# Kernel tuning notes

Measured on AMD Instinct MI355X. Metric: run time of the kernel, lower is better.

Reference implementation:

```python
import jax, jax.numpy as jnp
import numpy as np

N_NODES = 50000
N_EDGES = 800000
IN_FEAT = 128
OUT_FEAT = 128


def setup_inputs() -> dict:
    key = jax.random.key(0)
    k_h, k_src, k_dst, k_w, k_b = jax.random.split(key, 5)
    h = jax.random.normal(k_h, (N_NODES, IN_FEAT), dtype=jnp.float32)
    src = jax.random.randint(k_src, (N_EDGES,), 0, N_NODES, dtype=jnp.int64)
    dst = jax.random.randint(k_dst, (N_EDGES,), 0, N_NODES, dtype=jnp.int64)
    # nn.Linear(2*in_feat, out_feat): weight [out, 2*in], bias [out]
    W = jax.random.normal(k_w, (OUT_FEAT, 2 * IN_FEAT), dtype=jnp.float32) / np.sqrt(2 * IN_FEAT)
    b = jax.random.normal(k_b, (OUT_FEAT,), dtype=jnp.float32) * 0.01
    return {"h": h, "src": src, "dst": dst, "W": W, "b": b}


def reference(h, src, dst, W, b):
    n = h.shape[0]
    # copy_u + mean: gather source features per edge, mean-reduce by destination
    msg = h[src]  # [E, in_feat]
    agg = jax.ops.segment_sum(msg, dst, num_segments=n)  # [N, in_feat]
    deg = jax.ops.segment_sum(jnp.ones((dst.shape[0],), dtype=h.dtype), dst, num_segments=n)
    h_N = agg / jnp.maximum(deg, 1.0)[:, None]  # isolated nodes -> 0 (DGL mean semantics)
    h_total = jnp.concatenate([h, h_N], axis=1)  # [N, 2*in_feat]
    return h_total @ W.T + b
```

## Files before the change

kernel.cpp:

```cpp
#include <hip/hip_runtime.h>
#include <hip/hip_bf16.h>
#include <cstdint>
#include <cstddef>

#define NN     50000
#define NE     800000
#define FIN    128
#define CAP    64
#define NBIN   784
#define CAPBIN 1280
#define SB     157
#define SCT    1024
#define EPT    5
#define PREPB  786

using bf16x8 = __attribute__((ext_vector_type(8))) short;
using f32x4  = __attribute__((ext_vector_type(4))) float;
using f32x2  = __attribute__((ext_vector_type(2))) float;

static const size_t OFF_CUR  = 0;
static const size_t OFF_PART = 800;
static const size_t S_HB  = 2008640;
static const size_t S_HNB = 8408640;
static const size_t S_WB  = 14808640;
static const size_t S_HF8 = 14841408;

__device__ __forceinline__ unsigned f2bf(float f) {
    unsigned u = __float_as_uint(f);
    return (u + 0x7FFFu + ((u >> 16) & 1u)) >> 16;
}

__global__ __launch_bounds__(SCT) void k_ps(
    const float* __restrict__ h, const float* __restrict__ W,
    unsigned* __restrict__ hB, unsigned* __restrict__ WB,
    uint2* __restrict__ hF8,
    const int* __restrict__ src, const int* __restrict__ dst,
    int* __restrict__ bincursor, int* __restrict__ part)
{
    __shared__ int lcur[NBIN];
    __shared__ int lofs[NBIN];
    __shared__ int gbase[NBIN];
    __shared__ int wsum[16];
    __shared__ int ebuf[EPT * SCT];
    int blk = blockIdx.x, tid = threadIdx.x;

    if (blk >= SB) {
        int i = (blk - SB) * SCT + tid;
        size_t e = (size_t)i * 8;
        const float* s;
        unsigned* d;
        bool isH = (e < 6400000);
        if (isH) { s = h + e; d = hB + e / 2; }
        else if (e < 6400000 + 32768) { s = W + (e - 6400000); d = WB + (e - 6400000) / 2; }
        else return;
        float4 a = *(const float4*)s;
        float4 b = *(const float4*)(s + 4);
        uint4 o;
        o.x = f2bf(a.x) | (f2bf(a.y) << 16);
        o.y = f2bf(a.z) | (f2bf(a.w) << 16);
        o.z = f2bf(b.x) | (f2bf(b.y) << 16);
        o.w = f2bf(b.z) | (f2bf(b.w) << 16);
        *(uint4*)d = o;
        if (isH) {
            int w0 = __builtin_amdgcn_cvt_pk_fp8_f32(a.x, a.y, 0, false);
            w0     = __builtin_amdgcn_cvt_pk_fp8_f32(a.z, a.w, w0, true);
            int w1 = __builtin_amdgcn_cvt_pk_fp8_f32(b.x, b.y, 0, false);
            w1     = __builtin_amdgcn_cvt_pk_fp8_f32(b.z, b.w, w1, true);
            hF8[e / 8] = make_uint2((unsigned)w0, (unsigned)w1);
        }
        return;
    }

    int b = blk;
    if (tid < NBIN) lcur[tid] = 0;
    __syncthreads();
    int e0 = b * (EPT * SCT);
    int pk[EPT], rk[EPT];
#pragma unroll
    for (int k = 0; k < EPT; ++k) {
        int e = e0 + k * SCT + tid;
        if (e < NE) {
            int d = dst[e];
            int s = src[e];
            int bin = d >> 6;
            pk[k] = s | ((d & 63) << 16) | (bin << 22);
            rk[k] = atomicAdd(&lcur[bin], 1);
        } else {
            pk[k] = -1;
        }
    }
    __syncthreads();

    int lane = tid & 63, wid = tid >> 6;
    int c = (tid < NBIN) ? lcur[tid] : 0;
    int v = c;
#pragma unroll
    for (int dd = 1; dd < 64; dd <<= 1) {
        int n = __shfl_up(v, dd);
        if (lane >= dd) v += n;
    }
    if (lane == 63) wsum[wid] = v;
    __syncthreads();
    if (wid == 0) {
        int s16 = (lane < 16) ? wsum[lane] : 0;
        int wv = s16;
#pragma unroll
        for (int dd = 1; dd < 16; dd <<= 1) {
            int n = __shfl_up(wv, dd);
            if (lane >= dd) wv += n;
        }
        if (lane < 16) wsum[lane] = wv - s16;
    }
    __syncthreads();
    if (tid < NBIN) {
        lofs[tid]  = v - c + wsum[wid];
        gbase[tid] = c ? atomicAdd(&bincursor[tid], c) : 0;
    }
    __syncthreads();

#pragma unroll
    for (int k = 0; k < EPT; ++k) {
        if (pk[k] != -1) {
            int bin = ((unsigned)pk[k]) >> 22;
            ebuf[lofs[bin] + rk[k]] = pk[k];
        }
    }
    __syncthreads();

    int total = min(NE - e0, EPT * SCT);
    for (int i = tid; i < total; i += SCT) {
        int e = ebuf[i];
        int bin = ((unsigned)e) >> 22;
        int g = gbase[bin] + (i - lofs[bin]);
        if (g < CAPBIN)
            part[bin * CAPBIN + g] = e & 0x3FFFFF;
    }
}

__device__ __forceinline__ f32x2 fp8lo(unsigned u) {
    return __builtin_amdgcn_cvt_pk_f32_fp8((int)u, false);
}
__device__ __forceinline__ f32x2 fp8hi(unsigned u) {
    return __builtin_amdgcn_cvt_pk_f32_fp8((int)u, true);
}

__global__ __launch_bounds__(256) void k_aggbin(const int* __restrict__ part,
                                                const int* __restrict__ bincursor,
                                                const unsigned* __restrict__ hF8u,
                                                unsigned* __restrict__ hNB2) {
    __shared__ int ldeg[16];
    __shared__ unsigned short bucketL[16 * CAP];
    int blk = blockIdx.x, tid = threadIdx.x;
    int bin = blk >> 2, sub = blk & 3;
    if (tid < 16) ldeg[tid] = 0;
    __syncthreads();
    int cnt = min(bincursor[bin], CAPBIN);
    const int* pj = part + bin * CAPBIN;
    for (int i = tid; i < cnt; i += 256) {
        int v = pj[i];
        int local = (v >> 16) & 63;
        if ((local >> 4) == sub) {
            int l16 = local & 15;
            int slot = atomicAdd(&ldeg[l16], 1);
            if (slot < CAP) bucketL[l16 * CAP + slot] = (unsigned short)v;
        }
    }
    __syncthreads();
    int wave = tid >> 6, lane = tid & 63;
    int halfid = lane >> 5;
    int l32 = lane & 31;
#pragma unroll
    for (int t = 0; t < 4; ++t) {
        int l16 = wave * 4 + t;
        int n = bin * 64 + (sub << 4) + l16;
        if (n >= NN) continue;
        int d = ldeg[l16];
        int c2 = min(d, CAP);
        const unsigned short* bp = &bucketL[l16 * CAP];
        float a0 = 0.f, a1 = 0.f, a2 = 0.f, a3 = 0.f;
        int i = 0;
        for (; i + 16 <= c2; i += 16) {
            unsigned uu[8];
#pragma unroll
            for (int j = 0; j < 8; ++j)
                uu[j] = hF8u[(size_t)bp[i + 2 * j + halfid] * 32 + l32];
#pragma unroll
            for (int j = 0; j < 8; ++j) {
                f32x2 lo = fp8lo(uu[j]);
                f32x2 hi = fp8hi(uu[j]);
                a0 += lo[0]; a1 += lo[1]; a2 += hi[0]; a3 += hi[1];
            }
        }
        for (; i < c2; i += 2) {
            int e = i + halfid;
            unsigned u = 0;
            if (e < c2) u = hF8u[(size_t)bp[e] * 32 + l32];
            f32x2 lo = fp8lo(u);
            f32x2 hi = fp8hi(u);
            a0 += lo[0]; a1 += lo[1]; a2 += hi[0]; a3 += hi[1];
        }
        a0 += __shfl_xor(a0, 32);
        a1 += __shfl_xor(a1, 32);
        a2 += __shfl_xor(a2, 32);
        a3 += __shfl_xor(a3, 32);
        if (halfid == 0) {
            float inv = 1.0f / fmaxf((float)d, 1.0f);
            unsigned p0 = f2bf(a0 * inv) | (f2bf(a1 * inv) << 16);
            unsigned p1 = f2bf(a2 * inv) | (f2bf(a3 * inv) << 16);
            *(uint2*)(hNB2 + (size_t)n * 64 + l32 * 2) = make_uint2(p0, p1);
        }
    }
}

__global__ __launch_bounds__(256) void k_gemm(
    const short* __restrict__ hB, const short* __restrict__ hNB,
    const short* __restrict__ WB, const float* __restrict__ bias,
    float* __restrict__ out)
{
    __shared__ short WL[16384];
    const int tid = threadIdx.x;
    const int jbase = blockIdx.y * 64;

    for (int g = tid; g < 2048; g += 256) {
        int row = g >> 5;
        int c   = g & 31;
        int cs  = (c + row) & 31;
        bf16x8 v = *(const bf16x8*)(WB + (size_t)(jbase + row) * 256 + c * 8);
        *(bf16x8*)(&WL[row * 256 + cs * 8]) = v;
    }
    __syncthreads();

    const int wave = tid >> 6;
    const int lane = tid & 63;
    const int q    = lane >> 4;
    const int ln   = lane & 15;
    const int mbase = (blockIdx.x * 4 + wave) * 16;
    int node = mbase + ln;
    if (node >= NN) node = NN - 1;

    f32x4 acc[4];
#pragma unroll
    for (int t = 0; t < 4; ++t) acc[t] = (f32x4){0.f, 0.f, 0.f, 0.f};

#pragma unroll
    for (int k0 = 0; k0 < 8; ++k0) {
        int ck = k0 * 4 + q;
        const short* ap = (k0 < 4) ? (hB  + (size_t)node * 128 + ck * 8)
                                   : (hNB + (size_t)node * 128 + (ck - 16) * 8);
        bf16x8 afr = *(const bf16x8*)ap;
#pragma unroll
        for (int t = 0; t < 4; ++t) {
            int row = t * 16 + ln;
            int cs  = (ck + row) & 31;
            bf16x8 bfr = *(const bf16x8*)(&WL[row * 256 + cs * 8]);
            acc[t] = __builtin_amdgcn_mfma_f32_16x16x32_bf16(afr, bfr, acc[t], 0, 0, 0);
        }
    }

#pragma unroll
    for (int t = 0; t < 4; ++t) {
        float bv = bias[jbase + t * 16 + ln];
#pragma unroll
        for (int r = 0; r < 4; ++r) {
            int m = mbase + q * 4 + r;
            if (m < NN)
                out[(size_t)m * FIN + jbase + t * 16 + ln] = acc[t][r] + bv;
        }
    }
}

extern "C" void kernel_launch(void* const* d_in, const int* in_sizes, int n_in,
                              void* d_out, int out_size, void* d_ws, size_t ws_size,
                              hipStream_t stream) {
    const float* h   = (const float*)d_in[0];
    const int*   src = (const int*)d_in[1];
    const int*   dst = (const int*)d_in[2];
    const float* W   = (const float*)d_in[3];
    const float* b   = (const float*)d_in[4];
    float* out = (float*)d_out;

    int*   wsI = (int*)d_ws;
    short* wsS = (short*)d_ws;

    int* bincursor = wsI + OFF_CUR;
    int* part      = wsI + OFF_PART;
    short* hB      = wsS + S_HB;
    short* hNB     = wsS + S_HNB;
    short* WB      = wsS + S_WB;
    const unsigned* hF8u = (const unsigned*)(wsS + S_HF8);

    hipMemsetAsync(bincursor, 0, NBIN * sizeof(int), stream);
    k_ps     <<<SB + PREPB, SCT, 0, stream>>>(
        h, W, (unsigned*)hB, (unsigned*)WB, (uint2*)(wsS + S_HF8),
        src, dst, bincursor, part);
    k_aggbin <<<NBIN * 4, 256, 0, stream>>>(part, bincursor, hF8u, (unsigned*)hNB);
    k_gemm   <<<dim3((NN + 63) / 64, 2), 256, 0, stream>>>(hB, hNB, WB, b, out);
}
```

Before: 137.0 us.

## Fuse neighbor aggregation into GEMM kernel keeping mean features in LDS

Merges the binned aggregation kernel and the GEMM kernel into one kernel per 64-node bin. The aggregated neighbor means are written to a swizzled LDS tile instead of global memory and consumed directly as the second half of the A operand. This removes the hNB global round trip and one kernel launch. In exchange the grid shrinks from about 3136 aggregation blocks plus a 2-D GEMM grid to 782 blocks that each run four sequential sub-passes and reload W twice, which lowers parallelism and latency hiding for the gather.

New measurement: 187.6 us. 36.9% more time.

```diff
diff --git a/kernel.cpp b/kernel.cpp
--- a/kernel.cpp
+++ b/kernel.cpp
@@ -13,6 +13,7 @@
 #define SCT    1024
 #define EPT    5
 #define PREPB  786
+#define NAB    782
 
 using bf16x8 = __attribute__((ext_vector_type(8))) short;
 using f32x4  = __attribute__((ext_vector_type(4))) float;
@@ -144,127 +145,139 @@
     return __builtin_amdgcn_cvt_pk_f32_fp8((int)u, true);
 }
 
-__global__ __launch_bounds__(256) void k_aggbin(const int* __restrict__ part,
-                                                const int* __restrict__ bincursor,
-                                                const unsigned* __restrict__ hF8u,
-                                                unsigned* __restrict__ hNB2) {
-    __shared__ int ldeg[16];
-    __shared__ unsigned short bucketL[16 * CAP];
-    int blk = blockIdx.x, tid = threadIdx.x;
-    int bin = blk >> 2, sub = blk & 3;
-    if (tid < 16) ldeg[tid] = 0;
-    __syncthreads();
-    int cnt = min(bincursor[bin], CAPBIN);
-    const int* pj = part + bin * CAPBIN;
-    for (int i = tid; i < cnt; i += 256) {
-        int v = pj[i];
-        int local = (v >> 16) & 63;
-        if ((local >> 4) == sub) {
-            int l16 = local & 15;
-            int slot = atomicAdd(&ldeg[l16], 1);
-            if (slot < CAP) bucketL[l16 * CAP + slot] = (unsigned short)v;
-        }
-    }
-    __syncthreads();
-    int wave = tid >> 6, lane = tid & 63;
-    int halfid = lane >> 5;
-    int l32 = lane & 31;
-#pragma unroll
-    for (int t = 0; t < 4; ++t) {
-        int l16 = wave * 4 + t;
-        int n = bin * 64 + (sub << 4) + l16;
-        if (n >= NN) continue;
-        int d = ldeg[l16];
-        int c2 = min(d, CAP);
-        const unsigned short* bp = &bucketL[l16 * CAP];
-        float a0 = 0.f, a1 = 0.f, a2 = 0.f, a3 = 0.f;
-        int i = 0;
-        for (; i + 16 <= c2; i += 16) {
-            unsigned uu[8];
-#pragma unroll
-            for (int j = 0; j < 8; ++j)
-                uu[j] = hF8u[(size_t)bp[i + 2 * j + halfid] * 32 + l32];
-#pragma unroll
-            for (int j = 0; j < 8; ++j) {
-                f32x2 lo = fp8lo(uu[j]);
-                f32x2 hi = fp8hi(uu[j]);
-                a0 += lo[0]; a1 += lo[1]; a2 += hi[0]; a3 += hi[1];
-            }
-        }
-        for (; i < c2; i += 2) {
-            int e = i + halfid;
-            unsigned u = 0;
-            if (e < c2) u = hF8u[(size_t)bp[e] * 32 + l32];
-            f32x2 lo = fp8lo(u);
-            f32x2 hi = fp8hi(u);
-            a0 += lo[0]; a1 += lo[1]; a2 += hi[0]; a3 += hi[1];
-        }
-        a0 += __shfl_xor(a0, 32);
-        a1 += __shfl_xor(a1, 32);
-        a2 += __shfl_xor(a2, 32);
-        a3 += __shfl_xor(a3, 32);
-        if (halfid == 0) {
-            float inv = 1.0f / fmaxf((float)d, 1.0f);
-            unsigned p0 = f2bf(a0 * inv) | (f2bf(a1 * inv) << 16);
-            unsigned p1 = f2bf(a2 * inv) | (f2bf(a3 * inv) << 16);
-            *(uint2*)(hNB2 + (size_t)n * 64 + l32 * 2) = make_uint2(p0, p1);
-        }
-    }
-}
-
-__global__ __launch_bounds__(256) void k_gemm(
-    const short* __restrict__ hB, const short* __restrict__ hNB,
-    const short* __restrict__ WB, const float* __restrict__ bias,
+__global__ __launch_bounds__(256) void k_aggemm(
+    const int* __restrict__ part,
+    const int* __restrict__ bincursor,
+    const unsigned* __restrict__ hF8u,
+    const short* __restrict__ hB,
+    const short* __restrict__ WB,
+    const float* __restrict__ bias,
     float* __restrict__ out)
 {
     __shared__ short WL[16384];
-    const int tid = threadIdx.x;
-    const int jbase = blockIdx.y * 64;
-
-    for (int g = tid; g < 2048; g += 256) {
-        int row = g >> 5;
-        int c   = g & 31;
-        int cs  = (c + row) & 31;
-        bf16x8 v = *(const bf16x8*)(WB + (size_t)(jbase + row) * 256 + c * 8);
-        *(bf16x8*)(&WL[row * 256 + cs * 8]) = v;
-    }
-    __syncthreads();
-
-    const int wave = tid >> 6;
-    const int lane = tid & 63;
+    __shared__ short hNL[64 * 128];
+    __shared__ unsigned short bucketL[16 * CAP];
+    __shared__ int ldeg[16];
+
+    const int bin = blockIdx.x, tid = threadIdx.x;
+    const int wave = tid >> 6, lane = tid & 63;
+    const int halfid = lane >> 5;
+    const int l32 = lane & 31;
+
+    const int cnt = min(bincursor[bin], CAPBIN);
+    const int* pj = part + bin * CAPBIN;
+
+    for (int sub = 0; sub < 4; ++sub) {
+        if (tid < 16) ldeg[tid] = 0;
+        __syncthreads();
+        for (int i = tid; i < cnt; i += 256) {
+            int v = pj[i];
+            int local = (v >> 16) & 63;
+            if ((local >> 4) == sub) {
+                int l16 = local & 15;
+                int slot = atomicAdd(&ldeg[l16], 1);
+                if (slot < CAP) bucketL[l16 * CAP + slot] = (unsigned short)v;
+            }
+        }
+        __syncthreads();
+#pragma unroll
+        for (int t = 0; t < 4; ++t) {
+            int l16 = wave * 4 + t;
+            int row = (sub << 4) + l16;
+            int d = ldeg[l16];
+            int c2 = min(d, CAP);
+            const unsigned short* bp = &bucketL[l16 * CAP];
+            float a0 = 0.f, a1 = 0.f, a2 = 0.f, a3 = 0.f;
+            int i = 0;
+            for (; i + 16 <= c2; i += 16) {
+                unsigned uu[8];
+#pragma unroll
+                for (int j = 0; j < 8; ++j)
+                    uu[j] = hF8u[(size_t)bp[i + 2 * j + halfid] * 32 + l32];
+#pragma unroll
+                for (int j = 0; j < 8; ++j) {
+                    f32x2 lo = fp8lo(uu[j]);
+                    f32x2 hi = fp8hi(uu[j]);
+                    a0 += lo[0]; a1 += lo[1]; a2 += hi[0]; a3 += hi[1];
+                }
+            }
+            for (; i < c2; i += 2) {
+                int e = i + halfid;
+                unsigned u = 0;
+                if (e < c2) u = hF8u[(size_t)bp[e] * 32 + l32];
+                f32x2 lo = fp8lo(u);
+                f32x2 hi = fp8hi(u);
+                a0 += lo[0]; a1 += lo[1]; a2 += hi[0]; a3 += hi[1];
+            }
+            a0 += __shfl_xor(a0, 32);
+            a1 += __shfl_xor(a1, 32);
+            a2 += __shfl_xor(a2, 32);
+            a3 += __shfl_xor(a3, 32);
+            if (halfid == 0) {
+                float inv = 1.0f / fmaxf((float)d, 1.0f);
+                unsigned p0 = f2bf(a0 * inv) | (f2bf(a1 * inv) << 16);
+                unsigned p1 = f2bf(a2 * inv) | (f2bf(a3 * inv) << 16);
+                int c  = l32 >> 1;
+                int cs = (c + row) & 15;
+                *(uint2*)(&hNL[row * 128 + cs * 8 + (l32 & 1) * 4]) =
+                    make_uint2(p0, p1);
+            }
+        }
+        __syncthreads();
+    }
+
     const int q    = lane >> 4;
     const int ln   = lane & 15;
-    const int mbase = (blockIdx.x * 4 + wave) * 16;
-    int node = mbase + ln;
-    if (node >= NN) node = NN - 1;
-
-    f32x4 acc[4];
-#pragma unroll
-    for (int t = 0; t < 4; ++t) acc[t] = (f32x4){0.f, 0.f, 0.f, 0.f};
-
-#pragma unroll
-    for (int k0 = 0; k0 < 8; ++k0) {
-        int ck = k0 * 4 + q;
-        const short* ap = (k0 < 4) ? (hB  + (size_t)node * 128 + ck * 8)
-                                   : (hNB + (size_t)node * 128 + (ck - 16) * 8);
-        bf16x8 afr = *(const bf16x8*)ap;
+    const int mrow = wave * 16 + ln;
+    int node = bin * 64 + mrow;
+    int nodec = (node < NN) ? node : NN - 1;
+
+    for (int jh = 0; jh < 2; ++jh) {
+        const int jbase = jh * 64;
+        __syncthreads();
+        for (int g = tid; g < 2048; g += 256) {
+            int row = g >> 5;
+            int c   = g & 31;
+            int cs  = (c + row) & 31;
+            bf16x8 v = *(const bf16x8*)(WB + (size_t)(jbase + row) * 256 + c * 8);
+            *(bf16x8*)(&WL[row * 256 + cs * 8]) = v;
+        }
+        __syncthreads();
+
+        f32x4 acc[4];
+#pragma unroll
+        for (int t = 0; t < 4; ++t) acc[t] = (f32x4){0.f, 0.f, 0.f, 0.f};
+
+#pragma unroll
+        for (int k0 = 0; k0 < 8; ++k0) {
+            int ck = k0 * 4 + q;
+            bf16x8 afr;
+            if (k0 < 4) {
+                afr = *(const bf16x8*)(hB + (size_t)nodec * 128 + ck * 8);
+            } else {
+                int ckn = ck - 16;
+                int csn = (ckn + mrow) & 15;
+                afr = *(const bf16x8*)(&hNL[mrow * 128 + csn * 8]);
+            }
+#pragma unroll
+            for (int t = 0; t < 4; ++t) {
+                int row = t * 16 + ln;
+                int cs  = (ck + row) & 31;
+                bf16x8 bfr = *(const bf16x8*)(&WL[row * 256 + cs * 8]);
+                acc[t] = __builtin_amdgcn_mfma_f32_16x16x32_bf16(afr, bfr, acc[t], 0, 0, 0);
+            }
+        }
+
 #pragma unroll
         for (int t = 0; t < 4; ++t) {
-            int row = t * 16 + ln;
-            int cs  = (ck + row) & 31;
-            bf16x8 bfr = *(const bf16x8*)(&WL[row * 256 + cs * 8]);
-            acc[t] = __builtin_amdgcn_mfma_f32_16x16x32_bf16(afr, bfr, acc[t], 0, 0, 0);
-        }
-    }
-
-#pragma unroll
-    for (int t = 0; t < 4; ++t) {
-        float bv = bias[jbase + t * 16 + ln];
-#pragma unroll
-        for (int r = 0; r < 4; ++r) {
-            int m = mbase + q * 4 + r;
-            if (m < NN)
-                out[(size_t)m * FIN + jbase + t * 16 + ln] = acc[t][r] + bv;
+            int j = jbase + t * 16 + ln;
+            float bv = bias[j];
+#pragma unroll
+            for (int r = 0; r < 4; ++r) {
+                int m = bin * 64 + wave * 16 + q * 4 + r;
+                if (m < NN)
+                    out[(size_t)m * FIN + j] = acc[t][r] + bv;
+            }
         }
     }
 }
@@ -285,7 +298,6 @@
     int* bincursor = wsI + OFF_CUR;
     int* part      = wsI + OFF_PART;
     short* hB      = wsS + S_HB;
-    short* hNB     = wsS + S_HNB;
     short* WB      = wsS + S_WB;
     const unsigned* hF8u = (const unsigned*)(wsS + S_HF8);
 
@@ -293,6 +305,5 @@
     k_ps     <<<SB + PREPB, SCT, 0, stream>>>(
         h, W, (unsigned*)hB, (unsigned*)WB, (uint2*)(wsS + S_HF8),
         src, dst, bincursor, part);
-    k_aggbin <<<NBIN * 4, 256, 0, stream>>>(part, bincursor, hF8u, (unsigned*)hNB);
-    k_gemm   <<<dim3((NN + 63) / 64, 2), 256, 0, stream>>>(hB, hNB, WB, b, out);
-}
+    k_aggemm <<<NAB, 256, 0, stream>>>(part, bincursor, hF8u, hB, WB, b, out);
+}
```

## Replace global atomic bin cursors with per-block fixed segments in edge binning

Applied to the files above, without the earlier changes.

The partition step no longer reserves space in each destination bin through global atomicAdd on shared cursors. Instead, each scatter block writes its edges into a private fixed-size segment per bin and records its count, which also removes the memset of the cursors. The aggregation kernel then reads counts for all source blocks and scans every segment slot, skipping empty ones. This trades atomic contention and a memset for more, sparser global reads in aggregation, and edges past SEG per block-bin are silently dropped.

Result: slower. 150.7 us (+10.0%).

```diff
diff --git a/kernel.cpp b/kernel.cpp
--- a/kernel.cpp
+++ b/kernel.cpp
@@ -8,22 +8,22 @@
 #define FIN    128
 #define CAP    64
 #define NBIN   784
-#define CAPBIN 1280
 #define SB     157
 #define SCT    1024
 #define EPT    5
 #define PREPB  786
+#define SEG    32
 
 using bf16x8 = __attribute__((ext_vector_type(8))) short;
 using f32x4  = __attribute__((ext_vector_type(4))) float;
 using f32x2  = __attribute__((ext_vector_type(2))) float;
 
-static const size_t OFF_CUR  = 0;
-static const size_t OFF_PART = 800;
 static const size_t S_HB  = 2008640;
 static const size_t S_HNB = 8408640;
 static const size_t S_WB  = 14808640;
 static const size_t S_HF8 = 14841408;
+static const size_t OFF_PART2 = 10485760;
+static const size_t OFF_CNT2  = 15204352;
 
 __device__ __forceinline__ unsigned f2bf(float f) {
     unsigned u = __float_as_uint(f);
@@ -35,11 +35,10 @@
     unsigned* __restrict__ hB, unsigned* __restrict__ WB,
     uint2* __restrict__ hF8,
     const int* __restrict__ src, const int* __restrict__ dst,
-    int* __restrict__ bincursor, int* __restrict__ part)
+    int* __restrict__ part2, int* __restrict__ cnt2)
 {
     __shared__ int lcur[NBIN];
     __shared__ int lofs[NBIN];
-    __shared__ int gbase[NBIN];
     __shared__ int wsum[16];
     __shared__ int ebuf[EPT * SCT];
     int blk = blockIdx.x, tid = threadIdx.x;
@@ -113,8 +112,8 @@
     }
     __syncthreads();
     if (tid < NBIN) {
-        lofs[tid]  = v - c + wsum[wid];
-        gbase[tid] = c ? atomicAdd(&bincursor[tid], c) : 0;
+        lofs[tid] = v - c + wsum[wid];
+        cnt2[b * NBIN + tid] = min(c, SEG);
     }
     __syncthreads();
 
@@ -131,9 +130,9 @@
     for (int i = tid; i < total; i += SCT) {
         int e = ebuf[i];
         int bin = ((unsigned)e) >> 22;
-        int g = gbase[bin] + (i - lofs[bin]);
-        if (g < CAPBIN)
-            part[bin * CAPBIN + g] = e & 0x3FFFFF;
+        int r = i - lofs[bin];
+        if (r < SEG)
+            part2[((size_t)bin * SB + b) * SEG + r] = e & 0x3FFFFF;
     }
 }
 
@@ -144,25 +143,30 @@
     return __builtin_amdgcn_cvt_pk_f32_fp8((int)u, true);
 }
 
-__global__ __launch_bounds__(256) void k_aggbin(const int* __restrict__ part,
-                                                const int* __restrict__ bincursor,
+__global__ __launch_bounds__(256) void k_aggbin(const int* __restrict__ part2,
+                                                const int* __restrict__ cnt2,
                                                 const unsigned* __restrict__ hF8u,
                                                 unsigned* __restrict__ hNB2) {
     __shared__ int ldeg[16];
     __shared__ unsigned short bucketL[16 * CAP];
+    __shared__ int cblk[SB];
     int blk = blockIdx.x, tid = threadIdx.x;
     int bin = blk >> 2, sub = blk & 3;
     if (tid < 16) ldeg[tid] = 0;
-    __syncthreads();
-    int cnt = min(bincursor[bin], CAPBIN);
-    const int* pj = part + bin * CAPBIN;
-    for (int i = tid; i < cnt; i += 256) {
-        int v = pj[i];
-        int local = (v >> 16) & 63;
-        if ((local >> 4) == sub) {
-            int l16 = local & 15;
-            int slot = atomicAdd(&ldeg[l16], 1);
-            if (slot < CAP) bucketL[l16 * CAP + slot] = (unsigned short)v;
+    if (tid >= 64 && tid < 64 + SB) cblk[tid - 64] = cnt2[(tid - 64) * NBIN + bin];
+    __syncthreads();
+    const int* pj = part2 + (size_t)bin * SB * SEG;
+    for (int i = tid; i < SB * SEG; i += 256) {
+        int b = i >> 5;
+        int k = i & (SEG - 1);
+        if (k < cblk[b]) {
+            int v = pj[i];
+            int local = (v >> 16) & 63;
+            if ((local >> 4) == sub) {
+                int l16 = local & 15;
+                int slot = atomicAdd(&ldeg[l16], 1);
+                if (slot < CAP) bucketL[l16 * CAP + slot] = (unsigned short)v;
+            }
         }
     }
     __syncthreads();
@@ -282,17 +286,16 @@
     int*   wsI = (int*)d_ws;
     short* wsS = (short*)d_ws;
 
-    int* bincursor = wsI + OFF_CUR;
-    int* part      = wsI + OFF_PART;
-    short* hB      = wsS + S_HB;
-    short* hNB     = wsS + S_HNB;
-    short* WB      = wsS + S_WB;
+    int* part2 = wsI + OFF_PART2;
+    int* cnt2  = wsI + OFF_CNT2;
+    short* hB  = wsS + S_HB;
+    short* hNB = wsS + S_HNB;
+    short* WB  = wsS + S_WB;
     const unsigned* hF8u = (const unsigned*)(wsS + S_HF8);
 
-    hipMemsetAsync(bincursor, 0, NBIN * sizeof(int), stream);
     k_ps     <<<SB + PREPB, SCT, 0, stream>>>(
         h, W, (unsigned*)hB, (unsigned*)WB, (uint2*)(wsS + S_HF8),
-        src, dst, bincursor, part);
-    k_aggbin <<<NBIN * 4, 256, 0, stream>>>(part, bincursor, hF8u, (unsigned*)hNB);
+        src, dst, part2, cnt2);
+    k_aggbin <<<NBIN * 4, 256, 0, stream>>>(part2, cnt2, hF8u, (unsigned*)hNB);
     k_gemm   <<<dim3((NN + 63) / 64, 2), 256, 0, stream>>>(hB, hNB, WB, b, out);
 }
```
